# Performance work log

Hardware: AMD Instinct MI355X
Metric: run time of the kernel (lower is better)

The kernel has to match this reference:

```python
import jax, jax.numpy as jnp
import numpy as np

I, H, L = 128, 256, 64  # input_size, hidden_size, latent_dim
B, T = 64, 4096


def _lstm(x, h0, c0, Wih, Whh, bih, bhh):
    """x: [B,T,I]; returns (hs [B,T,H], hT [B,H]). PyTorch gate order i,f,g,o."""
    xg = jnp.einsum('bti,gi->btg', x, Wih) + bih  # precompute input projections

    def step(carry, xg_t):
        h, c = carry
        g = xg_t + h @ Whh.T + bhh
        i, f, gg, o = jnp.split(g, 4, axis=-1)
        c = jax.nn.sigmoid(f) * c + jax.nn.sigmoid(i) * jnp.tanh(gg)
        h = jax.nn.sigmoid(o) * jnp.tanh(c)
        return (h, c), h

    (hT, cT), hs = jax.lax.scan(step, (h0, c0), jnp.swapaxes(xg, 0, 1))
    return jnp.swapaxes(hs, 0, 1), hT


def setup_inputs() -> dict:
    key = jax.random.key(0)
    ks = jax.random.split(key, 20)
    s = 0.05
    d = {
        'padded_input': jax.random.normal(ks[0], (B, T, I), jnp.float32),
        'enc_Wih_f': jax.random.normal(ks[1], (4 * H, I), jnp.float32) * s,
        'enc_Whh_f': jax.random.normal(ks[2], (4 * H, H), jnp.float32) * s,
        'enc_bih_f': jax.random.normal(ks[3], (4 * H,), jnp.float32) * s,
        'enc_bhh_f': jax.random.normal(ks[4], (4 * H,), jnp.float32) * s,
        'enc_Wih_b': jax.random.normal(ks[5], (4 * H, I), jnp.float32) * s,
        'enc_Whh_b': jax.random.normal(ks[6], (4 * H, H), jnp.float32) * s,
        'enc_bih_b': jax.random.normal(ks[7], (4 * H,), jnp.float32) * s,
        'enc_bhh_b': jax.random.normal(ks[8], (4 * H,), jnp.float32) * s,
        'lat_W': jax.random.normal(ks[9], (L, 2 * H), jnp.float32) * s,
        'lat_b': jax.random.normal(ks[10], (L,), jnp.float32) * s,
        'l2h_W': jax.random.normal(ks[11], (H, L), jnp.float32) * s,
        'l2h_b': jax.random.normal(ks[12], (H,), jnp.float32) * s,
        'dec_Wih': jax.random.normal(ks[13], (4 * H, I), jnp.float32) * s,
        'dec_Whh': jax.random.normal(ks[14], (4 * H, H), jnp.float32) * s,
        'dec_bih': jax.random.normal(ks[15], (4 * H,), jnp.float32) * s,
        'dec_bhh': jax.random.normal(ks[16], (4 * H,), jnp.float32) * s,
        'out_W': jax.random.normal(ks[17], (I, H), jnp.float32) * s,
        'out_b': jax.random.normal(ks[18], (I,), jnp.float32) * s,
        'lengths': T,
    }
    return d


def reference(padded_input, enc_Wih_f, enc_Whh_f, enc_bih_f, enc_bhh_f,
              enc_Wih_b, enc_Whh_b, enc_bih_b, enc_bhh_b,
              lat_W, lat_b, l2h_W, l2h_b,
              dec_Wih, dec_Whh, dec_bih, dec_bhh, out_W, out_b, lengths):
    b = padded_input.shape[0]
    z = jnp.zeros((b, H), padded_input.dtype)
    # bidirectional encoder; only final hidden states are needed
    _, h_fwd = _lstm(padded_input, z, z, enc_Wih_f, enc_Whh_f, enc_bih_f, enc_bhh_f)
    _, h_bwd = _lstm(padded_input[:, ::-1], z, z, enc_Wih_b, enc_Whh_b, enc_bih_b, enc_bhh_b)
    h_n = jnp.concatenate([h_fwd, h_bwd], axis=1)  # [B, 2H]
    latent = h_n @ lat_W.T + lat_b                 # [B, L]
    hidden = latent @ l2h_W.T + l2h_b              # [B, H]
    # teacher forcing with ratio 1.0: decoder input at step t is padded_input[:, t-1]
    dec_in = padded_input[:, :-1]                  # [B, T-1, I]
    hs, _ = _lstm(dec_in, hidden, z, dec_Wih, dec_Whh, dec_bih, dec_bhh)
    decoded = jnp.einsum('bth,ih->bti', hs, out_W) + out_b  # [B, T-1, I]
    return decoded
```

## Files before the change

kernel.cpp:

```cpp
#include <hip/hip_runtime.h>
#include <stdint.h>

#define Ic 128
#define Hc 256

typedef uint32_t u32;
typedef unsigned long long u64;
using half2v = __attribute__((ext_vector_type(2))) _Float16;

__device__ __forceinline__ u32 pk_rne(float a, float b) {
    _Float16 lo = (_Float16)a, hi = (_Float16)b;
    return (u32)__builtin_bit_cast(uint16_t, lo) |
           ((u32)__builtin_bit_cast(uint16_t, hi) << 16);
}
__device__ __forceinline__ float dot2acc(u32 a, u32 b, float c) {
    return __builtin_amdgcn_fdot2(__builtin_bit_cast(half2v, a),
                                  __builtin_bit_cast(half2v, b), c, false);
}
__device__ __forceinline__ u32 rl(u32 v, int k) {
    return (u32)__builtin_amdgcn_readlane((int)v, k);
}
__device__ __forceinline__ float sigm(float x) {
    return __builtin_amdgcn_rcpf(1.f + __expf(-x));
}
__device__ __forceinline__ float tanh_f(float x) {
    float e = __expf(-2.f * __builtin_fabsf(x));
    float t = (1.f - e) * __builtin_amdgcn_rcpf(1.f + e);
    return __builtin_copysignf(t, x);
}
__device__ __forceinline__ u64 aload64(const u64* p) {
    return __hip_atomic_load(p, __ATOMIC_RELAXED, __HIP_MEMORY_SCOPE_AGENT);
}
__device__ __forceinline__ void astore64(u64* p, u64 v) {
    __hip_atomic_store(p, v, __ATOMIC_RELAXED, __HIP_MEMORY_SCOPE_AGENT);
}

__global__ __launch_bounds__(256, 1) void enc_kernel(
    const float* __restrict__ x,
    const float* __restrict__ WihF, const float* __restrict__ WhhF,
    const float* __restrict__ bihF, const float* __restrict__ bhhF,
    const float* __restrict__ WihB, const float* __restrict__ WhhB,
    const float* __restrict__ bihB, const float* __restrict__ bhhB,
    float* __restrict__ hF, float* __restrict__ hB,
    u64* __restrict__ xch,
    int T)
{
    const int t    = threadIdx.x;
    const int lane = t & 63;
    const int g    = blockIdx.x;
    const int half = (g >> 3) & 1;
    const int p    = ((g >> 4) << 3) | (g & 7);
    const int rev  = p >> 6;
    const int b    = p & 63;

    const int ug = t & 127;
    const int rA = (t >> 7) * Hc + half * 128 + ug;
    const int rB = ((t >> 7) + 2) * Hc + half * 128 + ug;

    const float* Wih = rev ? WihB : WihF;
    const float* Whh = rev ? WhhB : WhhF;
    const float* bih = rev ? bihB : bihF;
    const float* bhh = rev ? bhhB : bhhF;

    __shared__ u32   s_z[256];
    __shared__ float s_g[512];

    u32 whAo[64], whAp[64], wiA[64];
    u32 whBo[64], whBp[64], wiB[64];
    {
        const int ob = half * 64, pb2 = (half ^ 1) * 64;
        const float* wrA = Whh + (size_t)rA * Hc;
        const float* wrB = Whh + (size_t)rB * Hc;
#pragma unroll
        for (int j = 0; j < 64; j++) {
            whAo[j] = pk_rne(wrA[2*(ob+j)],  wrA[2*(ob+j)+1]);
            whBo[j] = pk_rne(wrB[2*(ob+j)],  wrB[2*(ob+j)+1]);
            whAp[j] = pk_rne(wrA[2*(pb2+j)], wrA[2*(pb2+j)+1]);
            whBp[j] = pk_rne(wrB[2*(pb2+j)], wrB[2*(pb2+j)+1]);
        }
        const float* irA = Wih + (size_t)rA * Ic;
        const float* irB = Wih + (size_t)rB * Ic;
#pragma unroll
        for (int j = 0; j < 64; j++) {
            wiA[j] = pk_rne(irA[2*j], irA[2*j+1]);
            wiB[j] = pk_rne(irB[2*j], irB[2*j+1]);
        }
    }
    const float biasA = bih[rA] + bhh[rA];
    const float biasB = bih[rB] + bhh[rB];

    const int own_off  = half * 64;
    const int peer_off = (half ^ 1) * 64;
    u64* xch_self = xch + ((size_t)(p * 2 + half)) * 128;
    u64* xch_peer = xch + ((size_t)(p * 2 + (half ^ 1))) * 128;

    if (t < 128) s_z[t] = 0u;
    if (t >= 128 && t < 192) {
        int m = t - 128;
        int ts0 = rev ? (T - 1) : 0;
        const float* xp = x + ((size_t)b * T + ts0) * Ic + 2 * m;
        s_z[128 + m] = pk_rne(xp[0], xp[1]);
    }
    if (t >= 192 && t < 256) {
        int m = t - 192;
        int ts1 = rev ? (T - 2) : 1;
        const float* xp = x + ((size_t)b * T + ts1) * Ic + 2 * m;
        s_z[192 + m] = pk_rne(xp[0], xp[1]);
    }
    __syncthreads();

    float c0 = 0.f, c1 = 0.f;
    for (int s = 0; s < T; s++) {
        u32 vzx = s_z[128 + (s & 1) * 64 + lane];
        u32 vzo = s_z[own_off + lane];
        float aA0 = biasA, aA1 = 0.f, aA2 = 0.f, aA3 = 0.f;
        float aB0 = biasB, aB1 = 0.f, aB2 = 0.f, aB3 = 0.f;
#pragma unroll
        for (int k = 0; k < 64; k += 4) {
            u32 h0 = rl(vzx, k+0), h1 = rl(vzx, k+1), h2 = rl(vzx, k+2), h3 = rl(vzx, k+3);
            aA0 = dot2acc(h0, wiA[k+0], aA0); aB0 = dot2acc(h0, wiB[k+0], aB0);
            aA1 = dot2acc(h1, wiA[k+1], aA1); aB1 = dot2acc(h1, wiB[k+1], aB1);
            aA2 = dot2acc(h2, wiA[k+2], aA2); aB2 = dot2acc(h2, wiB[k+2], aB2);
            aA3 = dot2acc(h3, wiA[k+3], aA3); aB3 = dot2acc(h3, wiB[k+3], aB3);
        }
#pragma unroll
        for (int k = 0; k < 64; k += 4) {
            u32 h0 = rl(vzo, k+0), h1 = rl(vzo, k+1), h2 = rl(vzo, k+2), h3 = rl(vzo, k+3);
            aA0 = dot2acc(h0, whAo[k+0], aA0); aB0 = dot2acc(h0, whBo[k+0], aB0);
            aA1 = dot2acc(h1, whAo[k+1], aA1); aB1 = dot2acc(h1, whBo[k+1], aB1);
            aA2 = dot2acc(h2, whAo[k+2], aA2); aB2 = dot2acc(h2, whBo[k+2], aB2);
            aA3 = dot2acc(h3, whAo[k+3], aA3); aB3 = dot2acc(h3, whBo[k+3], aB3);
        }
        if (s > 0 && (t >> 6) == 3) {
            u64 v;
            while ((int)((v = aload64(&xch_peer[(s & 1) * 64 + lane])) >> 32) < s)
                __builtin_amdgcn_s_sleep(1);
            s_z[peer_off + lane] = (u32)v;
        }
        __syncthreads();

        u32 vzp = s_z[peer_off + lane];
#pragma unroll
        for (int k = 0; k < 64; k += 4) {
            u32 h0 = rl(vzp, k+0), h1 = rl(vzp, k+1), h2 = rl(vzp, k+2), h3 = rl(vzp, k+3);
            aA0 = dot2acc(h0, whAp[k+0], aA0); aB0 = dot2acc(h0, whBp[k+0], aB0);
            aA1 = dot2acc(h1, whAp[k+1], aA1); aB1 = dot2acc(h1, whBp[k+1], aB1);
            aA2 = dot2acc(h2, whAp[k+2], aA2); aB2 = dot2acc(h2, whBp[k+2], aB2);
            aA3 = dot2acc(h3, whAp[k+3], aA3); aB3 = dot2acc(h3, whBp[k+3], aB3);
        }
        s_g[t]       = (aA0 + aA1) + (aA2 + aA3);
        s_g[t + 256] = (aB0 + aB1) + (aB2 + aB3);
        __syncthreads();

        const int notlast = (s + 1 < T);
        if (t < 64) {
            float i0 = s_g[2*t],     i1 = s_g[2*t+1];
            float f0 = s_g[128+2*t], f1 = s_g[128+2*t+1];
            float g0 = s_g[256+2*t], g1 = s_g[256+2*t+1];
            float o0 = s_g[384+2*t], o1 = s_g[384+2*t+1];
            c0 = sigm(f0)*c0 + sigm(i0)*tanh_f(g0);
            c1 = sigm(f1)*c1 + sigm(i1)*tanh_f(g1);
            float h0 = sigm(o0)*tanh_f(c0);
            float h1 = sigm(o1)*tanh_f(c1);
            u32 hp = pk_rne(h0, h1);
            s_z[own_off + t] = hp;
            if (notlast) {
                astore64(&xch_self[((s+1) & 1) * 64 + t],
                         ((u64)(u32)(s + 1) << 32) | (u64)hp);
            } else {
                float* ho = (rev ? hB : hF) + (size_t)b * Hc + half * 128 + 2 * t;
                ho[0] = h0; ho[1] = h1;
            }
        } else if (t < 128) {
            int sn = s + 2;
            if (sn < T) {
                int m = t - 64;
                int ts = rev ? (T - 1 - sn) : sn;
                const float* xp = x + ((size_t)b * T + ts) * Ic + 2 * m;
                s_z[128 + (sn & 1) * 64 + m] = pk_rne(xp[0], xp[1]);
            }
        }
        __syncthreads();
    }
}

__global__ void lat_kernel(const float* __restrict__ hF, const float* __restrict__ hB,
                           const float* __restrict__ latW, const float* __restrict__ latb,
                           const float* __restrict__ l2hW, const float* __restrict__ l2hb,
                           float* __restrict__ hidden)
{
    int b = blockIdx.x, t = threadIdx.x;
    __shared__ float s_hn[512];
    __shared__ float s_lat[64];
    s_hn[t]       = hF[(size_t)b * Hc + t];
    s_hn[256 + t] = hB[(size_t)b * Hc + t];
    __syncthreads();
    if (t < 64) {
        float a = latb[t];
        const float* wp = latW + (size_t)t * 512;
        for (int k = 0; k < 512; k++) a += wp[k] * s_hn[k];
        s_lat[t] = a;
    }
    __syncthreads();
    float a = l2hb[t];
    const float* wp = l2hW + (size_t)t * 64;
#pragma unroll
    for (int k = 0; k < 64; k++) a += wp[k] * s_lat[k];
    hidden[(size_t)b * Hc + t] = a;
}

__global__ __launch_bounds__(256, 1) void dec_kernel(
    const float* __restrict__ x,
    const float* __restrict__ Wih, const float* __restrict__ Whh,
    const float* __restrict__ bih, const float* __restrict__ bhh,
    const float* __restrict__ outW, const float* __restrict__ outb,
    const float* __restrict__ hidden, float* __restrict__ out,
    u64* __restrict__ xch,
    int T)
{
    const int t    = threadIdx.x;
    const int lane = t & 63;
    const int g    = blockIdx.x;
    const int half = (g >> 3) & 1;
    const int b    = ((g >> 4) << 3) | (g & 7);
    const int Ts   = T - 1;

    const int ug = t & 127;
    const int rA = (t >> 7) * Hc + half * 128 + ug;
    const int rB = ((t >> 7) + 2) * Hc + half * 128 + ug;

    __shared__ u32   s_z[256];
    __shared__ float s_g[512];
    __shared__ float s_op[256];
    __shared__ u32   s_ow[32 * 256];

    u32 whAo[64], whAp[64], wiA[64];
    u32 whBo[64], whBp[64], wiB[64];
    {
        const int ob = half * 64, pb2 = (half ^ 1) * 64;
        const float* wrA = Whh + (size_t)rA * Hc;
        const float* wrB = Whh + (size_t)rB * Hc;
#pragma unroll
        for (int j = 0; j < 64; j++) {
            whAo[j] = pk_rne(wrA[2*(ob+j)],  wrA[2*(ob+j)+1]);
            whBo[j] = pk_rne(wrB[2*(ob+j)],  wrB[2*(ob+j)+1]);
            whAp[j] = pk_rne(wrA[2*(pb2+j)], wrA[2*(pb2+j)+1]);
            whBp[j] = pk_rne(wrB[2*(pb2+j)], wrB[2*(pb2+j)+1]);
        }
        const float* irA = Wih + (size_t)rA * Ic;
        const float* irB = Wih + (size_t)rB * Ic;
#pragma unroll
        for (int j = 0; j < 64; j++) {
            wiA[j] = pk_rne(irA[2*j], irA[2*j+1]);
            wiB[j] = pk_rne(irB[2*j], irB[2*j+1]);
        }
    }
    const float biasA = bih[rA] + bhh[rA];
    const float biasB = bih[rB] + bhh[rB];

    {
        const float* op = outW + (size_t)(half * 64 + (t & 63)) * Hc + (size_t)(t >> 6) * 64;
#pragma unroll
        for (int j = 0; j < 32; j++)
            s_ow[j * 256 + t] = pk_rne(op[2*j], op[2*j+1]);
    }
    const float outb_r = (t >= 128 && t < 192) ? outb[half * 64 + (t - 128)] : 0.f;

    const int own_off  = half * 64;
    const int peer_off = (half ^ 1) * 64;
    u64* xch_self = xch + ((size_t)(b * 2 + half)) * 128;
    u64* xch_peer = xch + ((size_t)(b * 2 + (half ^ 1))) * 128;

    if (t < 128) {
        const float* hp = hidden + (size_t)b * Hc + 2 * t;
        s_z[t] = pk_rne(hp[0], hp[1]);
    }
    if (t >= 128 && t < 192) {
        int m = t - 128;
        const float* xp = x + ((size_t)b * T) * Ic + 2 * m;
        s_z[128 + m] = pk_rne(xp[0], xp[1]);
    }
    if (t >= 192 && t < 256) {
        int m = t - 192;
        const float* xp = x + ((size_t)b * T + 1) * Ic + 2 * m;
        s_z[192 + m] = pk_rne(xp[0], xp[1]);
    }
    __syncthreads();

    float c0 = 0.f, c1 = 0.f;
    for (int s = 0; s < Ts; s++) {
        u32 vzx = s_z[128 + (s & 1) * 64 + lane];
        u32 vzo = s_z[own_off + lane];
        float aA0 = biasA, aA1 = 0.f, aA2 = 0.f, aA3 = 0.f;
        float aB0 = biasB, aB1 = 0.f, aB2 = 0.f, aB3 = 0.f;
#pragma unroll
        for (int k = 0; k < 64; k += 4) {
            u32 h0 = rl(vzx, k+0), h1 = rl(vzx, k+1), h2 = rl(vzx, k+2), h3 = rl(vzx, k+3);
            aA0 = dot2acc(h0, wiA[k+0], aA0); aB0 = dot2acc(h0, wiB[k+0], aB0);
            aA1 = dot2acc(h1, wiA[k+1], aA1); aB1 = dot2acc(h1, wiB[k+1], aB1);
            aA2 = dot2acc(h2, wiA[k+2], aA2); aB2 = dot2acc(h2, wiB[k+2], aB2);
            aA3 = dot2acc(h3, wiA[k+3], aA3); aB3 = dot2acc(h3, wiB[k+3], aB3);
        }
#pragma unroll
        for (int k = 0; k < 64; k += 4) {
            u32 h0 = rl(vzo, k+0), h1 = rl(vzo, k+1), h2 = rl(vzo, k+2), h3 = rl(vzo, k+3);
            aA0 = dot2acc(h0, whAo[k+0], aA0); aB0 = dot2acc(h0, whBo[k+0], aB0);
            aA1 = dot2acc(h1, whAo[k+1], aA1); aB1 = dot2acc(h1, whBo[k+1], aB1);
            aA2 = dot2acc(h2, whAo[k+2], aA2); aB2 = dot2acc(h2, whBo[k+2], aB2);
            aA3 = dot2acc(h3, whAo[k+3], aA3); aB3 = dot2acc(h3, whBo[k+3], aB3);
        }
        if (s > 0 && (t >> 6) == 3) {
            u64 v;
            while ((int)((v = aload64(&xch_peer[(s & 1) * 64 + lane])) >> 32) < s)
                __builtin_amdgcn_s_sleep(1);
            s_z[peer_off + lane] = (u32)v;
        }
        __syncthreads();

        u32 vzp = s_z[peer_off + lane];
#pragma unroll
        for (int k = 0; k < 64; k += 4) {
            u32 h0 = rl(vzp, k+0), h1 = rl(vzp, k+1), h2 = rl(vzp, k+2), h3 = rl(vzp, k+3);
            aA0 = dot2acc(h0, whAp[k+0], aA0); aB0 = dot2acc(h0, whBp[k+0], aB0);
            aA1 = dot2acc(h1, whAp[k+1], aA1); aB1 = dot2acc(h1, whBp[k+1], aB1);
            aA2 = dot2acc(h2, whAp[k+2], aA2); aB2 = dot2acc(h2, whBp[k+2], aB2);
            aA3 = dot2acc(h3, whAp[k+3], aA3); aB3 = dot2acc(h3, whBp[k+3], aB3);
        }
        s_g[t]       = (aA0 + aA1) + (aA2 + aA3);
        s_g[t + 256] = (aB0 + aB1) + (aB2 + aB3);

        if (s > 0) {
            const int ksl = t >> 6;
            const int kb  = (ksl & 1) * 32;
            u32 vplo = s_z[lane];
            u32 vphi = s_z[64 + lane];
            float p0 = 0.f, p1 = 0.f;
#pragma unroll
            for (int j = 0; j < 32; j += 2) {
                u32 h0b = (ksl < 2) ? rl(vplo, kb + j)     : rl(vphi, kb + j);
                u32 h1b = (ksl < 2) ? rl(vplo, kb + j + 1) : rl(vphi, kb + j + 1);
                p0 = dot2acc(h0b, s_ow[(j)     * 256 + t], p0);
                p1 = dot2acc(h1b, s_ow[(j + 1) * 256 + t], p1);
            }
            s_op[(t & 63) * 4 + ksl] = p0 + p1;
        }
        __syncthreads();

        if (t < 64) {
            float i0 = s_g[2*t],     i1 = s_g[2*t+1];
            float f0 = s_g[128+2*t], f1 = s_g[128+2*t+1];
            float g0 = s_g[256+2*t], g1 = s_g[256+2*t+1];
            float o0 = s_g[384+2*t], o1 = s_g[384+2*t+1];
            c0 = sigm(f0)*c0 + sigm(i0)*tanh_f(g0);
            c1 = sigm(f1)*c1 + sigm(i1)*tanh_f(g1);
            float h0 = sigm(o0)*tanh_f(c0);
            float h1 = sigm(o1)*tanh_f(c1);
            u32 hp = pk_rne(h0, h1);
            s_z[own_off + t] = hp;
            astore64(&xch_self[((s+1) & 1) * 64 + t],
                     ((u64)(u32)(s + 1) << 32) | (u64)hp);
        } else if (t < 128) {
            int sn = s + 2;
            if (sn < Ts) {
                int m = t - 64;
                const float* xp = x + ((size_t)b * T + sn) * Ic + 2 * m;
                s_z[128 + (sn & 1) * 64 + m] = pk_rne(xp[0], xp[1]);
            }
        } else if (t < 192 && s > 0) {
            int rr = t - 128;
            float y = outb_r + ((s_op[rr*4+0] + s_op[rr*4+1]) + (s_op[rr*4+2] + s_op[rr*4+3]));
            out[((size_t)b * Ts + (s - 1)) * Ic + half * 64 + rr] = y;
        }
        __syncthreads();
    }

    if ((t >> 6) == 3) {
        u64 v;
        while ((int)((v = aload64(&xch_peer[(Ts & 1) * 64 + lane])) >> 32) < Ts)
            __builtin_amdgcn_s_sleep(1);
        s_z[peer_off + lane] = (u32)v;
    }
    __syncthreads();
    {
        const int ksl = t >> 6;
        const int kb  = (ksl & 1) * 32;
        u32 vplo = s_z[lane];
        u32 vphi = s_z[64 + lane];
        float p0 = 0.f, p1 = 0.f;
#pragma unroll
        for (int j = 0; j < 32; j += 2) {
            u32 h0b = (ksl < 2) ? rl(vplo, kb + j)     : rl(vphi, kb + j);
            u32 h1b = (ksl < 2) ? rl(vplo, kb + j + 1) : rl(vphi, kb + j + 1);
            p0 = dot2acc(h0b, s_ow[(j)     * 256 + t], p0);
            p1 = dot2acc(h1b, s_ow[(j + 1) * 256 + t], p1);
        }
        s_op[(t & 63) * 4 + ksl] = p0 + p1;
    }
    __syncthreads();
    if (t >= 128 && t < 192) {
        int rr = t - 128;
        float y = outb_r + ((s_op[rr*4+0] + s_op[rr*4+1]) + (s_op[rr*4+2] + s_op[rr*4+3]));
        out[((size_t)b * Ts + (Ts - 1)) * Ic + half * 64 + rr] = y;
    }
}

extern "C" void kernel_launch(void* const* d_in, const int* in_sizes, int n_in,
                              void* d_out, int out_size, void* d_ws, size_t ws_size,
                              hipStream_t stream)
{
    const float* x    = (const float*)d_in[0];
    const float* WihF = (const float*)d_in[1];
    const float* WhhF = (const float*)d_in[2];
    const float* bihF = (const float*)d_in[3];
    const float* bhhF = (const float*)d_in[4];
    const float* WihB = (const float*)d_in[5];
    const float* WhhB = (const float*)d_in[6];
    const float* bihB = (const float*)d_in[7];
    const float* bhhB = (const float*)d_in[8];
    const float* latW = (const float*)d_in[9];
    const float* latb = (const float*)d_in[10];
    const float* l2hW = (const float*)d_in[11];
    const float* l2hb = (const float*)d_in[12];
    const float* dWih = (const float*)d_in[13];
    const float* dWhh = (const float*)d_in[14];
    const float* dbih = (const float*)d_in[15];
    const float* dbhh = (const float*)d_in[16];
    const float* outW = (const float*)d_in[17];
    const float* outb = (const float*)d_in[18];

    const int T = in_sizes[0] / (64 * Ic);

    float* ws  = (float*)d_ws;
    float* hFp = ws;
    float* hBp = ws + 16384;
    float* hid = ws + 32768;
    u64* encXch = (u64*)(ws + 49152);
    u64* decXch = encXch + 32768;

    hipMemsetAsync(encXch, 0, (32768 + 16384) * sizeof(u64), stream);

    enc_kernel<<<256, 256, 0, stream>>>(x, WihF, WhhF, bihF, bhhF,
                                        WihB, WhhB, bihB, bhhB,
                                        hFp, hBp, encXch, T);
    lat_kernel<<<64, 256, 0, stream>>>(hFp, hBp, latW, latb, l2hW, l2hb, hid);
    dec_kernel<<<128, 256, 0, stream>>>(x, dWih, dWhh, dbih, dbhh,
                                        outW, outb, hid, (float*)d_out,
                                        decXch, T);
}
```

Before: 33.61 ms.

## Have every wave poll peer hidden state directly and drop a barrier per step

Each wave now loads the peer block's hidden-state slice straight from the global exchange buffer instead of waiting for one wave to copy it into shared memory. This removes one __syncthreads per timestep in both encoder and decoder, and the poll load is issued early so it overlaps the input and own-half dot products. In the decoder the output projection moves after the gate barrier and uses a double-buffered partial-sum array, so the output write is delayed one step and no longer adds work before the barrier. The cost is more global polling traffic, since all four waves spin on the flag instead of one.

```diff
diff --git a/kernel.cpp b/kernel.cpp
--- a/kernel.cpp
+++ b/kernel.cpp
@@ -62,7 +62,7 @@
     const float* bih = rev ? bihB : bihF;
     const float* bhh = rev ? bhhB : bhhF;
 
-    __shared__ u32   s_z[256];
+    __shared__ u32   s_z[192];
     __shared__ float s_g[512];
 
     u32 whAo[64], whAp[64], wiA[64];
@@ -89,30 +89,32 @@
     const float biasA = bih[rA] + bhh[rA];
     const float biasB = bih[rB] + bhh[rB];
 
-    const int own_off  = half * 64;
-    const int peer_off = (half ^ 1) * 64;
     u64* xch_self = xch + ((size_t)(p * 2 + half)) * 128;
     u64* xch_peer = xch + ((size_t)(p * 2 + (half ^ 1))) * 128;
 
-    if (t < 128) s_z[t] = 0u;
+    if (t < 64) s_z[t] = 0u;
+    if (t >= 64 && t < 128) {
+        int m = t - 64;
+        int ts0 = rev ? (T - 1) : 0;
+        const float* xp = x + ((size_t)b * T + ts0) * Ic + 2 * m;
+        s_z[64 + m] = pk_rne(xp[0], xp[1]);
+    }
     if (t >= 128 && t < 192) {
         int m = t - 128;
-        int ts0 = rev ? (T - 1) : 0;
-        const float* xp = x + ((size_t)b * T + ts0) * Ic + 2 * m;
-        s_z[128 + m] = pk_rne(xp[0], xp[1]);
-    }
-    if (t >= 192 && t < 256) {
-        int m = t - 192;
         int ts1 = rev ? (T - 2) : 1;
         const float* xp = x + ((size_t)b * T + ts1) * Ic + 2 * m;
-        s_z[192 + m] = pk_rne(xp[0], xp[1]);
+        s_z[128 + m] = pk_rne(xp[0], xp[1]);
     }
     __syncthreads();
 
     float c0 = 0.f, c1 = 0.f;
     for (int s = 0; s < T; s++) {
-        u32 vzx = s_z[128 + (s & 1) * 64 + lane];
-        u32 vzo = s_z[own_off + lane];
+        const u64* pslot = &xch_peer[(s & 1) * 64 + lane];
+        u64 pv = 0;
+        if (s > 0) pv = aload64(pslot);
+
+        u32 vzx = s_z[64 + (s & 1) * 64 + lane];
+        u32 vzo = s_z[lane];
         float aA0 = biasA, aA1 = 0.f, aA2 = 0.f, aA3 = 0.f;
         float aB0 = biasB, aB1 = 0.f, aB2 = 0.f, aB3 = 0.f;
 #pragma unroll
@@ -131,15 +133,14 @@
             aA2 = dot2acc(h2, whAo[k+2], aA2); aB2 = dot2acc(h2, whBo[k+2], aB2);
             aA3 = dot2acc(h3, whAo[k+3], aA3); aB3 = dot2acc(h3, whBo[k+3], aB3);
         }
-        if (s > 0 && (t >> 6) == 3) {
-            u64 v;
-            while ((int)((v = aload64(&xch_peer[(s & 1) * 64 + lane])) >> 32) < s)
+        u32 vzp = 0u;
+        if (s > 0) {
+            while ((u32)(pv >> 32) < (u32)s) {
                 __builtin_amdgcn_s_sleep(1);
-            s_z[peer_off + lane] = (u32)v;
-        }
-        __syncthreads();
-
-        u32 vzp = s_z[peer_off + lane];
+                pv = aload64(pslot);
+            }
+            vzp = (u32)pv;
+        }
 #pragma unroll
         for (int k = 0; k < 64; k += 4) {
             u32 h0 = rl(vzp, k+0), h1 = rl(vzp, k+1), h2 = rl(vzp, k+2), h3 = rl(vzp, k+3);
@@ -163,7 +164,7 @@
             float h0 = sigm(o0)*tanh_f(c0);
             float h1 = sigm(o1)*tanh_f(c1);
             u32 hp = pk_rne(h0, h1);
-            s_z[own_off + t] = hp;
+            s_z[t] = hp;
             if (notlast) {
                 astore64(&xch_self[((s+1) & 1) * 64 + t],
                          ((u64)(u32)(s + 1) << 32) | (u64)hp);
@@ -177,7 +178,7 @@
                 int m = t - 64;
                 int ts = rev ? (T - 1 - sn) : sn;
                 const float* xp = x + ((size_t)b * T + ts) * Ic + 2 * m;
-                s_z[128 + (sn & 1) * 64 + m] = pk_rne(xp[0], xp[1]);
+                s_z[64 + (sn & 1) * 64 + m] = pk_rne(xp[0], xp[1]);
             }
         }
         __syncthreads();
@@ -229,9 +230,9 @@
     const int rA = (t >> 7) * Hc + half * 128 + ug;
     const int rB = ((t >> 7) + 2) * Hc + half * 128 + ug;
 
-    __shared__ u32   s_z[256];
+    __shared__ u32   s_z[192];
     __shared__ float s_g[512];
-    __shared__ float s_op[256];
+    __shared__ float s_op[2][256];
     __shared__ u32   s_ow[32 * 256];
 
     u32 whAo[64], whAp[64], wiA[64];
@@ -266,31 +267,38 @@
     }
     const float outb_r = (t >= 128 && t < 192) ? outb[half * 64 + (t - 128)] : 0.f;
 
-    const int own_off  = half * 64;
-    const int peer_off = (half ^ 1) * 64;
     u64* xch_self = xch + ((size_t)(b * 2 + half)) * 128;
     u64* xch_peer = xch + ((size_t)(b * 2 + (half ^ 1))) * 128;
 
-    if (t < 128) {
-        const float* hp = hidden + (size_t)b * Hc + 2 * t;
+    if (t < 64) {
+        const float* hp = hidden + (size_t)b * Hc + half * 128 + 2 * t;
         s_z[t] = pk_rne(hp[0], hp[1]);
+    }
+    if (t >= 64 && t < 128) {
+        int m = t - 64;
+        const float* xp = x + ((size_t)b * T) * Ic + 2 * m;
+        s_z[64 + m] = pk_rne(xp[0], xp[1]);
     }
     if (t >= 128 && t < 192) {
         int m = t - 128;
-        const float* xp = x + ((size_t)b * T) * Ic + 2 * m;
+        const float* xp = x + ((size_t)b * T + 1) * Ic + 2 * m;
         s_z[128 + m] = pk_rne(xp[0], xp[1]);
     }
-    if (t >= 192 && t < 256) {
-        int m = t - 192;
-        const float* xp = x + ((size_t)b * T + 1) * Ic + 2 * m;
-        s_z[192 + m] = pk_rne(xp[0], xp[1]);
+    u32 vzp_init;
+    {
+        const float* hp = hidden + (size_t)b * Hc + (half ^ 1) * 128 + 2 * lane;
+        vzp_init = pk_rne(hp[0], hp[1]);
     }
     __syncthreads();
 
     float c0 = 0.f, c1 = 0.f;
     for (int s = 0; s < Ts; s++) {
-        u32 vzx = s_z[128 + (s & 1) * 64 + lane];
-        u32 vzo = s_z[own_off + lane];
+        const u64* pslot = &xch_peer[(s & 1) * 64 + lane];
+        u64 pv = 0;
+        if (s > 0) pv = aload64(pslot);
+
+        u32 vzx = s_z[64 + (s & 1) * 64 + lane];
+        u32 vzo = s_z[lane];
         float aA0 = biasA, aA1 = 0.f, aA2 = 0.f, aA3 = 0.f;
         float aB0 = biasB, aB1 = 0.f, aB2 = 0.f, aB3 = 0.f;
 #pragma unroll
@@ -309,15 +317,14 @@
             aA2 = dot2acc(h2, whAo[k+2], aA2); aB2 = dot2acc(h2, whBo[k+2], aB2);
             aA3 = dot2acc(h3, whAo[k+3], aA3); aB3 = dot2acc(h3, whBo[k+3], aB3);
         }
-        if (s > 0 && (t >> 6) == 3) {
-            u64 v;
-            while ((int)((v = aload64(&xch_peer[(s & 1) * 64 + lane])) >> 32) < s)
+        u32 vzp;
+        if (s > 0) {
+            while ((u32)(pv >> 32) < (u32)s) {
                 __builtin_amdgcn_s_sleep(1);
-            s_z[peer_off + lane] = (u32)v;
-        }
-        __syncthreads();
-
-        u32 vzp = s_z[peer_off + lane];
+                pv = aload64(pslot);
+            }
+            vzp = (u32)pv;
+        } else vzp = vzp_init;
 #pragma unroll
         for (int k = 0; k < 64; k += 4) {
             u32 h0 = rl(vzp, k+0), h1 = rl(vzp, k+1), h2 = rl(vzp, k+2), h3 = rl(vzp, k+3);
@@ -328,22 +335,6 @@
         }
         s_g[t]       = (aA0 + aA1) + (aA2 + aA3);
         s_g[t + 256] = (aB0 + aB1) + (aB2 + aB3);
-
-        if (s > 0) {
-            const int ksl = t >> 6;
-            const int kb  = (ksl & 1) * 32;
-            u32 vplo = s_z[lane];
-            u32 vphi = s_z[64 + lane];
-            float p0 = 0.f, p1 = 0.f;
-#pragma unroll
-            for (int j = 0; j < 32; j += 2) {
-                u32 h0b = (ksl < 2) ? rl(vplo, kb + j)     : rl(vphi, kb + j);
-                u32 h1b = (ksl < 2) ? rl(vplo, kb + j + 1) : rl(vphi, kb + j + 1);
-                p0 = dot2acc(h0b, s_ow[(j)     * 256 + t], p0);
-                p1 = dot2acc(h1b, s_ow[(j + 1) * 256 + t], p1);
-            }
-            s_op[(t & 63) * 4 + ksl] = p0 + p1;
-        }
         __syncthreads();
 
         if (t < 64) {
@@ -356,7 +347,7 @@
             float h0 = sigm(o0)*tanh_f(c0);
             float h1 = sigm(o1)*tanh_f(c1);
             u32 hp = pk_rne(h0, h1);
-            s_z[own_off + t] = hp;
+            s_z[t] = hp;
             astore64(&xch_self[((s+1) & 1) * 64 + t],
                      ((u64)(u32)(s + 1) << 32) | (u64)hp);
         } else if (t < 128) {
@@ -364,28 +355,51 @@
             if (sn < Ts) {
                 int m = t - 64;
                 const float* xp = x + ((size_t)b * T + sn) * Ic + 2 * m;
-                s_z[128 + (sn & 1) * 64 + m] = pk_rne(xp[0], xp[1]);
-            }
-        } else if (t < 192 && s > 0) {
+                s_z[64 + (sn & 1) * 64 + m] = pk_rne(xp[0], xp[1]);
+            }
+        } else if (t < 192 && s >= 2) {
             int rr = t - 128;
-            float y = outb_r + ((s_op[rr*4+0] + s_op[rr*4+1]) + (s_op[rr*4+2] + s_op[rr*4+3]));
-            out[((size_t)b * Ts + (s - 1)) * Ic + half * 64 + rr] = y;
+            const float* sp = s_op[(s - 1) & 1];
+            float y = outb_r + ((sp[rr*4+0] + sp[rr*4+1]) + (sp[rr*4+2] + sp[rr*4+3]));
+            out[((size_t)b * Ts + (s - 2)) * Ic + half * 64 + rr] = y;
+        }
+        if (s > 0) {
+            const int ksl = t >> 6;
+            const int kb  = (ksl & 1) * 32;
+            u32 vplo = half ? vzp : vzo;
+            u32 vphi = half ? vzo : vzp;
+            float p0 = 0.f, p1 = 0.f;
+#pragma unroll
+            for (int j = 0; j < 32; j += 2) {
+                u32 h0b = (ksl < 2) ? rl(vplo, kb + j)     : rl(vphi, kb + j);
+                u32 h1b = (ksl < 2) ? rl(vplo, kb + j + 1) : rl(vphi, kb + j + 1);
+                p0 = dot2acc(h0b, s_ow[(j)     * 256 + t], p0);
+                p1 = dot2acc(h1b, s_ow[(j + 1) * 256 + t], p1);
+            }
+            s_op[s & 1][(t & 63) * 4 + ksl] = p0 + p1;
         }
         __syncthreads();
     }
 
-    if ((t >> 6) == 3) {
-        u64 v;
-        while ((int)((v = aload64(&xch_peer[(Ts & 1) * 64 + lane])) >> 32) < Ts)
+    if (t >= 128 && t < 192) {
+        int rr = t - 128;
+        const float* sp = s_op[(Ts - 1) & 1];
+        float y = outb_r + ((sp[rr*4+0] + sp[rr*4+1]) + (sp[rr*4+2] + sp[rr*4+3]));
+        out[((size_t)b * Ts + (Ts - 2)) * Ic + half * 64 + rr] = y;
+    }
+    {
+        u32 vzo2 = s_z[lane];
+        const u64* pslot = &xch_peer[(Ts & 1) * 64 + lane];
+        u64 pv = aload64(pslot);
+        while ((u32)(pv >> 32) < (u32)Ts) {
             __builtin_amdgcn_s_sleep(1);
-        s_z[peer_off + lane] = (u32)v;
-    }
-    __syncthreads();
-    {
+            pv = aload64(pslot);
+        }
+        u32 vzp2 = (u32)pv;
         const int ksl = t >> 6;
         const int kb  = (ksl & 1) * 32;
-        u32 vplo = s_z[lane];
-        u32 vphi = s_z[64 + lane];
+        u32 vplo = half ? vzp2 : vzo2;
+        u32 vphi = half ? vzo2 : vzp2;
         float p0 = 0.f, p1 = 0.f;
 #pragma unroll
         for (int j = 0; j < 32; j += 2) {
@@ -394,12 +408,13 @@
             p0 = dot2acc(h0b, s_ow[(j)     * 256 + t], p0);
             p1 = dot2acc(h1b, s_ow[(j + 1) * 256 + t], p1);
         }
-        s_op[(t & 63) * 4 + ksl] = p0 + p1;
+        s_op[Ts & 1][(t & 63) * 4 + ksl] = p0 + p1;
     }
     __syncthreads();
     if (t >= 128 && t < 192) {
         int rr = t - 128;
-        float y = outb_r + ((s_op[rr*4+0] + s_op[rr*4+1]) + (s_op[rr*4+2] + s_op[rr*4+3]));
+        const float* sp = s_op[Ts & 1];
+        float y = outb_r + ((sp[rr*4+0] + sp[rr*4+1]) + (sp[rr*4+2] + sp[rr*4+3]));
         out[((size_t)b * Ts + (Ts - 1)) * Ic + half * 64 + rr] = y;
     }
 }
```

After: 30.37 ms. 9.6% less time.
